# Performance work log

Hardware: AMD Instinct MI355X
Metric: run time of the kernel (lower is better)

Reference implementation:

```python
import jax, jax.numpy as jnp
import numpy as np
from jax import lax

EMBED_DIM = 128
HIDDEN = 50
KS = 7
BN_EPS = 1e-5


def setup_inputs() -> dict:
    key = jax.random.key(0)
    ks = jax.random.split(key, 8)
    B, L, D, H = 4, 512, EMBED_DIM, HIDDEN
    x1 = jax.random.normal(ks[0], (B, L, D), jnp.float32)
    x2 = jax.random.normal(ks[1], (B, L, D), jnp.float32)
    # conv1 (1x1) weight stored as [H, 2D] (spatial dims of size 1 dropped)
    conv1_w = jax.random.normal(ks[2], (H, 2 * D), jnp.float32) * (1.0 / np.sqrt(2 * D))
    conv1_b = jnp.zeros((H,), jnp.float32)
    bn1_g = jnp.ones((H,), jnp.float32)
    bn1_b = jnp.zeros((H,), jnp.float32)
    w2 = jax.random.normal(ks[3], (1, H, KS, KS), jnp.float32) * (1.0 / np.sqrt(H * KS * KS))
    conv2_w = 0.5 * (w2 + jnp.swapaxes(w2, 2, 3))  # clip(): symmetrize kernel
    conv2_b = jnp.zeros((1,), jnp.float32)
    bn2_g = jnp.ones((1,), jnp.float32)
    bn2_b = jnp.zeros((1,), jnp.float32)
    return {"x1": x1, "x2": x2, "conv1_w": conv1_w, "conv1_b": conv1_b,
            "bn1_g": bn1_g, "bn1_b": bn1_b, "conv2_w": conv2_w, "conv2_b": conv2_b,
            "bn2_g": bn2_g, "bn2_b": bn2_b}


def _batch_norm(x, g, b):
    # train-mode BN: batch statistics over (N, H, W), biased variance (PyTorch)
    m = jnp.mean(x, axis=(0, 2, 3), keepdims=True)
    v = jnp.var(x, axis=(0, 2, 3), keepdims=True)
    xn = (x - m) * lax.rsqrt(v + BN_EPS)
    return xn * g[None, :, None, None] + b[None, :, None, None]


def reference(x1, x2, conv1_w, conv1_b, bn1_g, bn1_b, conv2_w, conv2_b, bn2_g, bn2_b):
    # x1, x2: [B, L, D] -> channel-first [B, D, L]
    x1c = jnp.swapaxes(x1, 1, 2)
    x2c = jnp.swapaxes(x2, 1, 2)
    D = x1c.shape[1]
    w_dif, w_mul = conv1_w[:, :D], conv1_w[:, D:]
    # 1x1 conv over concat([|x1_i - x2_j|, x1_i * x2_j]) fused as two contractions
    dif = jnp.abs(x1c[:, :, :, None] - x2c[:, :, None, :])        # [B, D, L1, L2]
    h = jnp.einsum('bdij,hd->bhij', dif, w_dif)
    h = h + jnp.einsum('bdi,bdj,hd->bhij', x1c, x2c, w_mul)       # mul term, no [B,D,L,L] materialized by hand
    h = h + conv1_b[None, :, None, None]
    h = jax.nn.relu(h)                 # activation1 BEFORE batch_norm1 (as in source)
    h = _batch_norm(h, bn1_g, bn1_b)
    # conv2: symmetric 7x7, padding ks//2 == SAME for odd ks
    y = lax.conv_general_dilated(h, conv2_w, window_strides=(1, 1), padding='SAME',
                                 dimension_numbers=('NCHW', 'OIHW', 'NCHW'))
    y = y + conv2_b[None, :, None, None]
    y = _batch_norm(y, bn2_g, bn2_b)
    y = jax.nn.sigmoid(y)
    return y[:, 0, :, :]               # squeeze channel -> [B, L1, L2]
```

## Files before the change

### kernel.cpp

```cpp
#include <hip/hip_runtime.h>

#define LL 512
#define DD 128
#define HH 50
#define JW 520

typedef short v8s __attribute__((ext_vector_type(8)));
typedef float f32x4 __attribute__((ext_vector_type(4)));
typedef float f32x2 __attribute__((ext_vector_type(2)));
typedef unsigned int u32x4 __attribute__((ext_vector_type(4)));

__device__ __forceinline__ unsigned cvtpk(float a, float b) {
  unsigned r;
  asm("v_cvt_pk_bf16_f32 %0, %1, %2" : "=v"(r) : "v"(a), "v"(b));
  return r;
}
__device__ __forceinline__ unsigned cvtpkabs(float a, float b) {
  unsigned r;
  asm("v_cvt_pk_bf16_f32 %0, abs(%1), abs(%2)" : "=v"(r) : "v"(a), "v"(b));
  return r;
}
__device__ __forceinline__ unsigned short f2bf(float f) {
  unsigned u = __builtin_bit_cast(unsigned, f);
  u = (u + 0x7fffu + ((u >> 16) & 1u)) >> 16;
  return (unsigned short)u;
}
__device__ __forceinline__ void gload16(const void* g, void* l) {
  __builtin_amdgcn_global_load_lds(
      (const __attribute__((address_space(1))) unsigned int*)g,
      (__attribute__((address_space(3))) unsigned int*)l, 16, 0, 0);
}

__global__ void pass0(const float* __restrict__ c1w, unsigned short* __restrict__ wbuf)
{
  const int idx = blockIdx.x * 256 + threadIdx.x;
  const int r = idx >> 8, c = idx & 255;
  wbuf[(r << 8) | (c ^ ((r & 7) << 3))] = f2bf((r < HH) ? c1w[idx] : 0.f);
}

__global__ __launch_bounds__(256, 2) void pass1(
    const float* __restrict__ x1, const float* __restrict__ x2,
    const unsigned short* __restrict__ wbuf, const float* __restrict__ c1b,
    unsigned short* __restrict__ hbuf, float* __restrict__ partials)
{
  __shared__ unsigned short wlin[64 * 256];
  __shared__ float x1s[16 * 128];

  const int tid = threadIdx.x;
  const int wv = tid >> 6, lane = tid & 63;
  const int lh = lane & 15, lg = lane >> 4;
  const int bx = blockIdx.x, by = blockIdx.y, bz = blockIdx.z;
  const int j0 = bx << 6, i0 = by << 4;

#pragma unroll
  for (int k = 0; k < 8; ++k)
    gload16(wbuf + (((k << 8) + tid) << 3), wlin + ((((k << 2) + wv) << 6) << 3));
  {
    const float* x1base = x1 + (size_t)(bz * LL + i0) * DD;
#pragma unroll
    for (int k = 0; k < 2; ++k)
      gload16(x1base + (((k << 8) + tid) << 2), x1s + ((((k << 2) + wv) << 6) << 2));
  }
  __syncthreads();

  v8s bfr[4][8];
  {
    const unsigned wbase = (unsigned)(size_t)
        ((__attribute__((address_space(3))) char*)&wlin[0]);
#pragma unroll
    for (int n = 0; n < 4; n++)
#pragma unroll
      for (int kt = 0; kt < 8; kt++) {
        const int row = n * 16 + lh;
        const int col = (kt * 32 + lg * 8) ^ ((row & 7) << 3);
        unsigned off = wbase + (unsigned)(((row << 8) + col) << 1);
        asm volatile("ds_read_b128 %0, %1" : "=v"(bfr[n][kt]) : "v"(off));
      }
    asm volatile("s_waitcnt lgkmcnt(0)" ::: "memory");
    __builtin_amdgcn_sched_barrier(0);
  }

  f32x2 x2p[4][4];
  {
    const int j = j0 + (wv << 4) + lh;
    const float* g = x2 + ((size_t)(bz * LL + j) * DD + (lg << 3));
#pragma unroll
    for (int kt = 0; kt < 4; kt++)
#pragma unroll
      for (int m = 0; m < 4; m++)
        x2p[kt][m] = *(const f32x2*)(g + kt * 32 + 2 * m);
  }
  f32x2 bias2[4][2];
#pragma unroll
  for (int n = 0; n < 4; n++)
#pragma unroll
    for (int h2 = 0; h2 < 2; h2++) {
      int h0 = n * 16 + (lg << 2) + 2 * h2;
      bias2[n][h2] = f32x2{(h0 < HH) ? c1b[h0] : 0.f,
                           (h0 + 1 < HH) ? c1b[h0 + 1] : 0.f};
    }

  f32x2 ssum2[4][2], ssq2[4][2];
#pragma unroll
  for (int n = 0; n < 4; n++)
#pragma unroll
    for (int h2 = 0; h2 < 2; h2++) {
      ssum2[n][h2] = f32x2{0.f, 0.f};
      ssq2[n][h2] = f32x2{0.f, 0.f};
    }

  unsigned short* hb = hbuf +
      ((size_t)(bz * LL + i0) * JW + 4 + j0 + (wv << 4) + lh) * 64 + (lg << 2);

#pragma unroll 2
  for (int di = 0; di < 16; ++di) {
    f32x4 acc[4];
#pragma unroll
    for (int n = 0; n < 4; n++) acc[n] = f32x4{0.f, 0.f, 0.f, 0.f};
#pragma unroll
    for (int kt = 0; kt < 4; ++kt) {
      const float* xr = &x1s[(di << 7) + kt * 32 + (lg << 3)];
      u32x4 ad, am;
#pragma unroll
      for (int m = 0; m < 4; m++) {
        f32x2 xp = *(const f32x2*)(xr + 2 * m);
        f32x2 d = xp - x2p[kt][m];
        f32x2 pr = xp * x2p[kt][m];
        ad[m] = cvtpkabs(d[0], d[1]);
        am[m] = cvtpk(pr[0], pr[1]);
      }
      v8s vad = __builtin_bit_cast(v8s, ad);
      v8s vam = __builtin_bit_cast(v8s, am);
#pragma unroll
      for (int n = 0; n < 4; n++)
        acc[n] = __builtin_amdgcn_mfma_f32_16x16x32_bf16(bfr[n][kt], vad, acc[n], 0, 0, 0);
#pragma unroll
      for (int n = 0; n < 4; n++)
        acc[n] = __builtin_amdgcn_mfma_f32_16x16x32_bf16(bfr[n][kt + 4], vam, acc[n], 0, 0, 0);
    }
    unsigned short* hp = hb + (size_t)di * (JW * 64);
#pragma unroll
    for (int n = 0; n < 4; ++n) {
      f32x2 v0 = f32x2{acc[n][0], acc[n][1]} + bias2[n][0];
      f32x2 v1 = f32x2{acc[n][2], acc[n][3]} + bias2[n][1];
      v0 = __builtin_elementwise_max(v0, f32x2{0.f, 0.f});
      v1 = __builtin_elementwise_max(v1, f32x2{0.f, 0.f});
      ssum2[n][0] += v0; ssum2[n][1] += v1;
      ssq2[n][0] += v0 * v0; ssq2[n][1] += v1 * v1;
      unsigned lo = cvtpk(v0[0], v0[1]), hi = cvtpk(v1[0], v1[1]);
      *(unsigned long long*)(hp + n * 16) = ((unsigned long long)hi << 32) | lo;
    }
  }

  __syncthreads();
  float* stred = x1s;
#pragma unroll
  for (int n = 0; n < 4; ++n)
#pragma unroll
    for (int q = 0; q < 4; ++q) {
      float s = ssum2[n][q >> 1][q & 1], t = ssq2[n][q >> 1][q & 1];
#pragma unroll
      for (int m = 1; m < 16; m <<= 1) { s += __shfl_xor(s, m); t += __shfl_xor(t, m); }
      if (lh == 0) {
        stred[(wv << 7) + n * 16 + (lg << 2) + q] = s;
        stred[(wv << 7) + 64 + n * 16 + (lg << 2) + q] = t;
      }
    }
  __syncthreads();
  if (tid < 128) {
    int bid = (bz * gridDim.y + by) * gridDim.x + bx;
    partials[bid * 128 + tid] = stred[tid] + stred[128 + tid] + stred[256 + tid] + stred[384 + tid];
  }

  if (bx == 0 || bx == 7) {
    const int jb = (bx == 0) ? 0 : 516;
#pragma unroll
    for (int k = 0; k < 2; ++k) {
      int unit = tid + (k << 8);
      int ii = unit >> 5;
      int rem = unit & 31;
      int jj = jb + (rem >> 3);
      int ch = (rem & 7) << 3;
      u32x4 z = {0u, 0u, 0u, 0u};
      *(u32x4*)&hbuf[((size_t)(bz * LL + i0 + ii) * JW + jj) * 64 + ch] = z;
    }
  }
}

__global__ void pass2a(const float* __restrict__ partials, float* __restrict__ red1)
{
  __shared__ float acc2[2][128];
  const int tid = threadIdx.x, b = blockIdx.x;
  const int slot = tid & 127, half = tid >> 7;
  float s = 0.f;
#pragma unroll
  for (int k = 0; k < 8; k++)
    s += partials[(b * 16 + half * 8 + k) * 128 + slot];
  acc2[half][slot] = s;
  __syncthreads();
  if (tid < 128) red1[b * 128 + tid] = acc2[0][tid] + acc2[1][tid];
}

__global__ void pass2b(const float* __restrict__ red1,
                       const float* __restrict__ c2w, const float* __restrict__ c2b,
                       const float* __restrict__ bn1g, const float* __restrict__ bn1b,
                       unsigned short* __restrict__ wA, float* __restrict__ tmap)
{
  __shared__ float acc2[2][128];
  __shared__ float sq[128];
  __shared__ float aa[64], cc[64];
  __shared__ float wlds[2450];
  __shared__ float tpart[49][5];
  const int tid = threadIdx.x;
  const int slot = tid & 127, half = tid >> 7;
  float s = 0.f;
#pragma unroll
  for (int k = 0; k < 32; k++) s += red1[(half * 32 + k) * 128 + slot];
  acc2[half][slot] = s;
  __syncthreads();
  if (tid < 128) sq[tid] = acc2[0][tid] + acc2[1][tid];
  for (int i = tid; i < 2450; i += 256) wlds[i] = c2w[i];
  __syncthreads();
  if (tid < HH) {
    float S = sq[tid], Q = sq[64 + tid];
    const float N = 4.0f * 512.f * 512.f;
    float m = S / N, v = fmaxf(Q / N - m * m, 0.f);
    float a = bn1g[tid] * rsqrtf(v + 1e-5f);
    aa[tid] = a;
    cc[tid] = bn1b[tid] - m * a;
  }
  __syncthreads();
  for (int idx = tid; idx < 16 * 448; idx += 256) {
    int ky = idx / 448, r = idx - ky * 448;
    int kx = r >> 6, ch = r & 63;
    float v = (ky < 7 && ch < HH) ? aa[ch] * wlds[ch * 49 + ky * 7 + kx] : 0.f;
    wA[idx] = f2bf(v);
  }
  if (tid < 245) {
    int c = tid / 5, g = tid - (tid / 5) * 5;
    int ci = c / 7, cj = c - (c / 7) * 7;
    int kylo = ci < 3 ? 3 - ci : 0, kyhi = ci > 3 ? 9 - ci : 6;
    int kxlo = cj < 3 ? 3 - cj : 0, kxhi = cj > 3 ? 9 - cj : 6;
    float t = 0.f;
    for (int h = g * 10; h < g * 10 + 10; h++) {
      float sm = 0.f;
      for (int ky = kylo; ky <= kyhi; ky++)
        for (int kx = kxlo; kx <= kxhi; kx++) sm += wlds[h * 49 + ky * 7 + kx];
      t += cc[h] * sm;
    }
    tpart[c][g] = t;
  }
  __syncthreads();
  if (tid < 49)
    tmap[tid] = c2b[0] + tpart[tid][0] + tpart[tid][1] + tpart[tid][2]
              + tpart[tid][3] + tpart[tid][4];
}

__global__ __launch_bounds__(256, 4) void pass3(
    const unsigned short* __restrict__ hbuf, const unsigned short* __restrict__ wA,
    const float* __restrict__ tmap, float* __restrict__ ybuf, float* __restrict__ part2)
{
  __shared__ unsigned short T[2][72 * 64];
  __shared__ float tm[49];
  __shared__ float rs[4], rq[4];

  const int tid = threadIdx.x;
  const int wv = tid >> 6, lane = tid & 63;
  const int lh = lane & 15, lg = lane >> 4;
  const int bx = blockIdx.x, by = blockIdx.y, bz = blockIdx.z;
  const int j0 = bx << 6, i0 = by << 4;

  v8s afr[14];
#pragma unroll
  for (int kt = 0; kt < 14; kt++)
    afr[kt] = *(const v8s*)&wA[lh * 448 + kt * 32 + (lg << 3)];

  if (tid < 49) tm[tid] = tmap[tid];

  const int jc = (wv << 4) + lh;
  float ya[4] = {0.f, 0.f, 0.f, 0.f};

  auto stage = [&](int buf, int row) {
    const unsigned short* rowp = hbuf + ((size_t)(bz * LL + row) * JW + j0) * 64;
#pragma unroll
    for (int cc2 = 0; cc2 < 2; ++cc2) {
      const int c = wv + (cc2 << 2);
      const int u = (c << 6) + lane;
      const int tj = u >> 3, oct = u & 7;
      gload16(rowp + tj * 64 + ((oct ^ (tj & 7)) << 3), &T[buf][c << 9]);
    }
    if (wv == 0) {
      const int u = 512 + lane;
      const int tj = u >> 3, oct = u & 7;
      gload16(rowp + tj * 64 + ((oct ^ (tj & 7)) << 3), &T[buf][8 << 9]);
    }
  };

  { const int r0 = i0 - 3; if (r0 >= 0) stage(0, r0); }
  __syncthreads();

  for (int rb = 0; rb < 24; rb += 8) {
#pragma unroll
    for (int u8 = 0; u8 < 8; ++u8) {
      const int rr = rb + u8;
      const int r = i0 - 3 + rr;
      const int cur = rr & 1;
      if (rr + 1 < 22) {
        const int rn = r + 1;
        if (rn >= 0 && rn < LL) stage(cur ^ 1, rn);
      }
      if (rr < 22 && r >= 0 && r < LL) {
        f32x4 a0 = {0.f, 0.f, 0.f, 0.f}, a1 = {0.f, 0.f, 0.f, 0.f};
#pragma unroll
        for (int kt = 0; kt < 14; ++kt) {
          const int kx = kt >> 1;
          const int t = jc + 1 + kx;
          const int sl = ((kt & 1) << 2) + lg;
          v8s b = *(const v8s*)&T[cur][(t << 6) + ((sl ^ (t & 7)) << 3)];
          if (kt & 1) a1 = __builtin_amdgcn_mfma_f32_16x16x32_bf16(afr[kt], b, a1, 0, 0, 0);
          else        a0 = __builtin_amdgcn_mfma_f32_16x16x32_bf16(afr[kt], b, a0, 0, 0, 0);
        }
        float zq[4];
#pragma unroll
        for (int q = 0; q < 4; ++q) zq[q] = a0[q] + a1[q];
#pragma unroll
        for (int ky = 0; ky < 7; ++ky) {
          float zz = __shfl(zq[ky & 3], ((ky >> 2) << 4) + lh, 64);
          const int idx = rr - ky;
          const bool ok = ((unsigned)idx < 16u) && ((idx >> 2) == lg);
          ya[(u8 - ky) & 3] += ok ? zz : 0.f;
        }
      }
      __syncthreads();
    }
  }

  float sa = 0.f, qa = 0.f;
  const int jj = j0 + jc;
  const int cj = jj < 3 ? jj : (jj > 508 ? jj - 505 : 3);
#pragma unroll
  for (int s = 0; s < 4; ++s) {
    const int i = i0 + (lg << 2) + s;
    const int ci = i < 3 ? i : (i > 508 ? i - 505 : 3);
    float v = ya[s] + tm[ci * 7 + cj];
    ybuf[(size_t)(bz * LL + i) * LL + jj] = v;
    sa += v; qa += v * v;
  }
#pragma unroll
  for (int m = 1; m < 64; m <<= 1) { sa += __shfl_xor(sa, m); qa += __shfl_xor(qa, m); }
  if (lane == 0) { rs[wv] = sa; rq[wv] = qa; }
  __syncthreads();
  if (tid == 0) {
    const int bid = (bz * gridDim.y + by) * gridDim.x + bx;
    part2[bid] = rs[0] + rs[1] + rs[2] + rs[3];
    part2[1024 + bid] = rq[0] + rq[1] + rq[2] + rq[3];
  }
}

__global__ void pass3b(const float* __restrict__ part2, float* __restrict__ stats2)
{
  __shared__ float rs[4], rq[4];
  const int tid = threadIdx.x;
  float s = 0.f, q = 0.f;
  for (int i = tid; i < 1024; i += 256) { s += part2[i]; q += part2[1024 + i]; }
#pragma unroll
  for (int m = 1; m < 64; m <<= 1) { s += __shfl_xor(s, m); q += __shfl_xor(q, m); }
  const int wave = tid >> 6, lane = tid & 63;
  if (lane == 0) { rs[wave] = s; rq[wave] = q; }
  __syncthreads();
  if (tid == 0) {
    float S = rs[0] + rs[1] + rs[2] + rs[3];
    float Q = rq[0] + rq[1] + rq[2] + rq[3];
    const float N = 4.0f * 512.f * 512.f;
    float m2 = S / N, v2 = fmaxf(Q / N - m2 * m2, 0.f);
    stats2[0] = m2;
    stats2[1] = rsqrtf(v2 + 1e-5f);
  }
}

__global__ void pass4(const float* __restrict__ y, const float* __restrict__ stats2,
                      const float* __restrict__ bn2g, const float* __restrict__ bn2b,
                      float* __restrict__ out)
{
  const int idx = blockIdx.x * 256 + threadIdx.x;
  const float m2 = stats2[0], inv = stats2[1];
  const float g = bn2g[0], b = bn2b[0];
  f32x4 v = ((const f32x4*)y)[idx];
  f32x4 r;
#pragma unroll
  for (int e = 0; e < 4; e++) {
    float xn = (v[e] - m2) * inv * g + b;
    r[e] = 1.f / (1.f + __expf(-xn));
  }
  ((f32x4*)out)[idx] = r;
}

extern "C" void kernel_launch(void* const* d_in, const int* in_sizes, int n_in,
                              void* d_out, int out_size, void* d_ws, size_t ws_size,
                              hipStream_t stream) {
  (void)in_sizes; (void)n_in; (void)out_size; (void)ws_size;
  const float* x1   = (const float*)d_in[0];
  const float* x2   = (const float*)d_in[1];
  const float* c1w  = (const float*)d_in[2];
  const float* c1b  = (const float*)d_in[3];
  const float* bn1g = (const float*)d_in[4];
  const float* bn1b = (const float*)d_in[5];
  const float* c2w  = (const float*)d_in[6];
  const float* c2b  = (const float*)d_in[7];
  const float* bn2g = (const float*)d_in[8];
  const float* bn2b = (const float*)d_in[9];

  char* ws = (char*)d_ws;
  float* partials       = (float*)(ws + 0);
  float* red1           = (float*)(ws + 524288);
  float* part2          = (float*)(ws + 557056);
  unsigned short* wA    = (unsigned short*)(ws + 565248);
  float* tmap           = (float*)(ws + 579584);
  float* stats2         = (float*)(ws + 579840);
  unsigned short* wbuf  = (unsigned short*)(ws + 581632);
  float* ybuf           = (float*)(ws + 1048576);
  unsigned short* hbuf  = (unsigned short*)(ws + 5242880);

  pass0<<<64, 256, 0, stream>>>(c1w, wbuf);
  pass1<<<dim3(8, 32, 4), 256, 0, stream>>>(x1, x2, wbuf, c1b, hbuf, partials);
  pass2a<<<64, 256, 0, stream>>>(partials, red1);
  pass2b<<<1, 256, 0, stream>>>(red1, c2w, c2b, bn1g, bn1b, wA, tmap);
  pass3<<<dim3(8, 32, 4), 256, 0, stream>>>(hbuf, wA, tmap, ybuf, part2);
  pass3b<<<1, 256, 0, stream>>>(part2, stats2);
  pass4<<<1024, 256, 0, stream>>>(ybuf, stats2, bn2g, bn2b, (float*)d_out);
}
```

Before: 125.9 us.

## Split pass1 hidden channels across wave pairs and double grid width

Each pass1 block now covers 32 j columns instead of 64, with pairs of waves splitting the 64 hidden channels in half. Per-wave register use for weight fragments, accumulators and stats drops by half, and the grid doubles to 2048 blocks. The partials reduction and pass2a are adjusted to match, and the partials buffer moves to an offset shared with ybuf because it is now larger. The cost is that every block repeats the weight and x1 loads into LDS, and the x2 conversion work is done twice per j.

Result: slower. 134.1 us (+6.5%).

```diff
diff --git a/kernel.cpp b/kernel.cpp
--- a/kernel.cpp
+++ b/kernel.cpp
@@ -49,8 +49,9 @@
   const int tid = threadIdx.x;
   const int wv = tid >> 6, lane = tid & 63;
   const int lh = lane & 15, lg = lane >> 4;
+  const int jg = wv >> 1, nh = wv & 1;
   const int bx = blockIdx.x, by = blockIdx.y, bz = blockIdx.z;
-  const int j0 = bx << 6, i0 = by << 4;
+  const int j0 = bx << 5, i0 = by << 4;
 
 #pragma unroll
   for (int k = 0; k < 8; ++k)
@@ -63,18 +64,18 @@
   }
   __syncthreads();
 
-  v8s bfr[4][8];
+  v8s bfr[2][8];
   {
     const unsigned wbase = (unsigned)(size_t)
         ((__attribute__((address_space(3))) char*)&wlin[0]);
 #pragma unroll
-    for (int n = 0; n < 4; n++)
+    for (int n2 = 0; n2 < 2; n2++)
 #pragma unroll
       for (int kt = 0; kt < 8; kt++) {
-        const int row = n * 16 + lh;
+        const int row = nh * 32 + n2 * 16 + lh;
         const int col = (kt * 32 + lg * 8) ^ ((row & 7) << 3);
         unsigned off = wbase + (unsigned)(((row << 8) + col) << 1);
-        asm volatile("ds_read_b128 %0, %1" : "=v"(bfr[n][kt]) : "v"(off));
+        asm volatile("ds_read_b128 %0, %1" : "=v"(bfr[n2][kt]) : "v"(off));
       }
     asm volatile("s_waitcnt lgkmcnt(0)" ::: "memory");
     __builtin_amdgcn_sched_barrier(0);
@@ -82,7 +83,7 @@
 
   f32x2 x2p[4][4];
   {
-    const int j = j0 + (wv << 4) + lh;
+    const int j = j0 + (jg << 4) + lh;
     const float* g = x2 + ((size_t)(bz * LL + j) * DD + (lg << 3));
 #pragma unroll
     for (int kt = 0; kt < 4; kt++)
@@ -90,33 +91,33 @@
       for (int m = 0; m < 4; m++)
         x2p[kt][m] = *(const f32x2*)(g + kt * 32 + 2 * m);
   }
-  f32x2 bias2[4][2];
-#pragma unroll
-  for (int n = 0; n < 4; n++)
+  f32x2 bias2[2][2];
+#pragma unroll
+  for (int n2 = 0; n2 < 2; n2++)
 #pragma unroll
     for (int h2 = 0; h2 < 2; h2++) {
-      int h0 = n * 16 + (lg << 2) + 2 * h2;
-      bias2[n][h2] = f32x2{(h0 < HH) ? c1b[h0] : 0.f,
-                           (h0 + 1 < HH) ? c1b[h0 + 1] : 0.f};
-    }
-
-  f32x2 ssum2[4][2], ssq2[4][2];
-#pragma unroll
-  for (int n = 0; n < 4; n++)
+      int h0 = nh * 32 + n2 * 16 + (lg << 2) + 2 * h2;
+      bias2[n2][h2] = f32x2{(h0 < HH) ? c1b[h0] : 0.f,
+                            (h0 + 1 < HH) ? c1b[h0 + 1] : 0.f};
+    }
+
+  f32x2 ssum2[2][2], ssq2[2][2];
+#pragma unroll
+  for (int n2 = 0; n2 < 2; n2++)
 #pragma unroll
     for (int h2 = 0; h2 < 2; h2++) {
-      ssum2[n][h2] = f32x2{0.f, 0.f};
-      ssq2[n][h2] = f32x2{0.f, 0.f};
+      ssum2[n2][h2] = f32x2{0.f, 0.f};
+      ssq2[n2][h2] = f32x2{0.f, 0.f};
     }
 
   unsigned short* hb = hbuf +
-      ((size_t)(bz * LL + i0) * JW + 4 + j0 + (wv << 4) + lh) * 64 + (lg << 2);
+      ((size_t)(bz * LL + i0) * JW + 4 + j0 + (jg << 4) + lh) * 64 + nh * 32 + (lg << 2);
 
 #pragma unroll 2
   for (int di = 0; di < 16; ++di) {
-    f32x4 acc[4];
-#pragma unroll
-    for (int n = 0; n < 4; n++) acc[n] = f32x4{0.f, 0.f, 0.f, 0.f};
+    f32x4 acc[2];
+#pragma unroll
+    for (int n2 = 0; n2 < 2; n2++) acc[n2] = f32x4{0.f, 0.f, 0.f, 0.f};
 #pragma unroll
     for (int kt = 0; kt < 4; ++kt) {
       const float* xr = &x1s[(di << 7) + kt * 32 + (lg << 3)];
@@ -132,47 +133,50 @@
       v8s vad = __builtin_bit_cast(v8s, ad);
       v8s vam = __builtin_bit_cast(v8s, am);
 #pragma unroll
-      for (int n = 0; n < 4; n++)
-        acc[n] = __builtin_amdgcn_mfma_f32_16x16x32_bf16(bfr[n][kt], vad, acc[n], 0, 0, 0);
-#pragma unroll
-      for (int n = 0; n < 4; n++)
-        acc[n] = __builtin_amdgcn_mfma_f32_16x16x32_bf16(bfr[n][kt + 4], vam, acc[n], 0, 0, 0);
+      for (int n2 = 0; n2 < 2; n2++)
+        acc[n2] = __builtin_amdgcn_mfma_f32_16x16x32_bf16(bfr[n2][kt], vad, acc[n2], 0, 0, 0);
+#pragma unroll
+      for (int n2 = 0; n2 < 2; n2++)
+        acc[n2] = __builtin_amdgcn_mfma_f32_16x16x32_bf16(bfr[n2][kt + 4], vam, acc[n2], 0, 0, 0);
     }
     unsigned short* hp = hb + (size_t)di * (JW * 64);
 #pragma unroll
-    for (int n = 0; n < 4; ++n) {
-      f32x2 v0 = f32x2{acc[n][0], acc[n][1]} + bias2[n][0];
-      f32x2 v1 = f32x2{acc[n][2], acc[n][3]} + bias2[n][1];
+    for (int n2 = 0; n2 < 2; ++n2) {
+      f32x2 v0 = f32x2{acc[n2][0], acc[n2][1]} + bias2[n2][0];
+      f32x2 v1 = f32x2{acc[n2][2], acc[n2][3]} + bias2[n2][1];
       v0 = __builtin_elementwise_max(v0, f32x2{0.f, 0.f});
       v1 = __builtin_elementwise_max(v1, f32x2{0.f, 0.f});
-      ssum2[n][0] += v0; ssum2[n][1] += v1;
-      ssq2[n][0] += v0 * v0; ssq2[n][1] += v1 * v1;
+      ssum2[n2][0] += v0; ssum2[n2][1] += v1;
+      ssq2[n2][0] += v0 * v0; ssq2[n2][1] += v1 * v1;
       unsigned lo = cvtpk(v0[0], v0[1]), hi = cvtpk(v1[0], v1[1]);
-      *(unsigned long long*)(hp + n * 16) = ((unsigned long long)hi << 32) | lo;
+      *(unsigned long long*)(hp + n2 * 16) = ((unsigned long long)hi << 32) | lo;
     }
   }
 
   __syncthreads();
   float* stred = x1s;
 #pragma unroll
-  for (int n = 0; n < 4; ++n)
+  for (int n2 = 0; n2 < 2; ++n2)
 #pragma unroll
     for (int q = 0; q < 4; ++q) {
-      float s = ssum2[n][q >> 1][q & 1], t = ssq2[n][q >> 1][q & 1];
+      float s = ssum2[n2][q >> 1][q & 1], t = ssq2[n2][q >> 1][q & 1];
 #pragma unroll
       for (int m = 1; m < 16; m <<= 1) { s += __shfl_xor(s, m); t += __shfl_xor(t, m); }
       if (lh == 0) {
-        stred[(wv << 7) + n * 16 + (lg << 2) + q] = s;
-        stred[(wv << 7) + 64 + n * 16 + (lg << 2) + q] = t;
+        stred[(wv << 6) + n2 * 16 + (lg << 2) + q] = s;
+        stred[(wv << 6) + 32 + n2 * 16 + (lg << 2) + q] = t;
       }
     }
   __syncthreads();
   if (tid < 128) {
+    const int is_sq = tid >> 6, ch = tid & 63;
+    const int nh2 = ch >> 5, cl = ch & 31;
+    const int idx = is_sq * 32 + cl;
     int bid = (bz * gridDim.y + by) * gridDim.x + bx;
-    partials[bid * 128 + tid] = stred[tid] + stred[128 + tid] + stred[256 + tid] + stred[384 + tid];
-  }
-
-  if (bx == 0 || bx == 7) {
+    partials[bid * 128 + tid] = stred[(nh2 << 6) + idx] + stred[((2 + nh2) << 6) + idx];
+  }
+
+  if (bx == 0 || bx == 15) {
     const int jb = (bx == 0) ? 0 : 516;
 #pragma unroll
     for (int k = 0; k < 2; ++k) {
@@ -194,8 +198,8 @@
   const int slot = tid & 127, half = tid >> 7;
   float s = 0.f;
 #pragma unroll
-  for (int k = 0; k < 8; k++)
-    s += partials[(b * 16 + half * 8 + k) * 128 + slot];
+  for (int k = 0; k < 16; k++)
+    s += partials[(b * 32 + half * 16 + k) * 128 + slot];
   acc2[half][slot] = s;
   __syncthreads();
   if (tid < 128) red1[b * 128 + tid] = acc2[0][tid] + acc2[1][tid];
@@ -411,18 +415,18 @@
   const float* bn2b = (const float*)d_in[9];
 
   char* ws = (char*)d_ws;
-  float* partials       = (float*)(ws + 0);
   float* red1           = (float*)(ws + 524288);
   float* part2          = (float*)(ws + 557056);
   unsigned short* wA    = (unsigned short*)(ws + 565248);
   float* tmap           = (float*)(ws + 579584);
   float* stats2         = (float*)(ws + 579840);
   unsigned short* wbuf  = (unsigned short*)(ws + 581632);
+  float* partials       = (float*)(ws + 1048576);
   float* ybuf           = (float*)(ws + 1048576);
   unsigned short* hbuf  = (unsigned short*)(ws + 5242880);
 
   pass0<<<64, 256, 0, stream>>>(c1w, wbuf);
-  pass1<<<dim3(8, 32, 4), 256, 0, stream>>>(x1, x2, wbuf, c1b, hbuf, partials);
+  pass1<<<dim3(16, 32, 4), 256, 0, stream>>>(x1, x2, wbuf, c1b, hbuf, partials);
   pass2a<<<64, 256, 0, stream>>>(partials, red1);
   pass2b<<<1, 256, 0, stream>>>(red1, c2w, c2b, bn1g, bn1b, wA, tmap);
   pass3<<<dim3(8, 32, 4), 256, 0, stream>>>(hbuf, wA, tmap, ybuf, part2);
```
